# Kernel tuning notes

Hardware: AMD Instinct MI355X
Metric: run time of the kernel (lower is better)

The kernel has to match this reference:

```python
import jax, jax.numpy as jnp
import numpy as np

B, S, H, D = 2, 2048, 16, 64


def setup_inputs() -> dict:
    key = jax.random.key(0)
    kq, kk, kv, km = jax.random.split(key, 4)
    q = jax.random.normal(kq, (B, S, H, D), dtype=jnp.float32)
    k = jax.random.normal(kk, (B, S, H, D), dtype=jnp.float32)
    v = jax.random.normal(kv, (B, S, H, D), dtype=jnp.float32)
    key_padding_mask = jax.random.randint(km, (B, S), 0, 2).astype(bool)
    return {"q": q, "k": k, "v": v, "key_padding_mask": key_padding_mask}


def reference(q, k, v, key_padding_mask):
    # [B,S,H,D] -> [B,H,S,D]; fp32 upcast (inputs already fp32)
    qt = jnp.transpose(q, (0, 2, 1, 3)).astype(jnp.float32)
    kt = jnp.transpose(k, (0, 2, 1, 3)).astype(jnp.float32)
    vt = jnp.transpose(v, (0, 2, 1, 3)).astype(jnp.float32)
    scale = D ** (-0.5)
    # [B,H,Sq,Sk]
    scores = jnp.einsum("bhqd,bhkd->bhqk", qt, kt) * scale
    # masked_fill where key_padding_mask is True -> -inf
    mask = key_padding_mask[:, None, None, :]  # [B,1,1,Sk]
    scores = jnp.where(mask, -jnp.inf, scores)
    attn = jax.nn.softmax(scores, axis=-1)
    out = jnp.einsum("bhqk,bhkd->bhqd", attn, vt).astype(q.dtype)
    # back to [B,S,H,D]
    return jnp.transpose(out, (0, 2, 1, 3))
```

## Files before the change

kernel.cpp:

```cpp
#include <hip/hip_runtime.h>
#include <hip/hip_bf16.h>

#define BB 2
#define SS 2048
#define HH 16
#define DD 64
#define BR 128
#define BC 64
#define NT (SS / BC)
#define NQT (SS / BR)
#define TILE_E (BC * DD)
#define LOG2E 1.44269504f
#define LSTR 72

typedef __attribute__((ext_vector_type(8))) short short8;
typedef __attribute__((ext_vector_type(4))) float f32x4;
typedef __attribute__((ext_vector_type(16))) float f32x16;
typedef __attribute__((ext_vector_type(4))) unsigned int uint32x4;
typedef __attribute__((ext_vector_type(4))) unsigned short ushort4_t;

static __device__ __forceinline__ unsigned short f2bf(float f) {
    unsigned int u = __float_as_uint(f);
    unsigned int r = u + 0x7FFFu + ((u >> 16) & 1u);
    return (unsigned short)(r >> 16);
}
static __device__ __forceinline__ unsigned int pack2(float a, float b) {
    return (unsigned int)f2bf(a) | ((unsigned int)f2bf(b) << 16);
}
static __device__ __forceinline__ float fexp2(float x) {
#if __has_builtin(__builtin_amdgcn_exp2f)
    return __builtin_amdgcn_exp2f(x);
#else
    return exp2f(x);
#endif
}
static __device__ __forceinline__ void gl_lds16(const void* g, void* l) {
    __builtin_amdgcn_global_load_lds(
        (const __attribute__((address_space(1))) void*)g,
        (__attribute__((address_space(3))) void*)l, 16, 0, 0);
}

__global__ __launch_bounds__(256, 2)
void prep_kernel(const float* __restrict__ K, const float* __restrict__ V,
                 const int* __restrict__ M,
                 unsigned short* __restrict__ Kb, unsigned short* __restrict__ Vt,
                 unsigned long long* __restrict__ Mb64)
{
    __shared__ unsigned short Vl[DD * LSTR];

    const int t  = blockIdx.x & (NT - 1);
    const int b  = blockIdx.x >> 9;
    const int bh = blockIdx.x >> 5;
    const int tid = threadIdx.x;
    const size_t tile = (size_t)blockIdx.x * TILE_E;
    const size_t rs = (size_t)HH * DD;
    const float* kb0 = K + (((size_t)b * SS + t * BC) * HH + (bh & 15)) * DD;
    const float* vb0 = V + (((size_t)b * SS + t * BC) * HH + (bh & 15)) * DD;

    {
        const int p  = tid & 7;
        const int r0 = tid >> 3;
        #pragma unroll
        for (int half = 0; half < 2; ++half) {
            const int r = r0 + half * 32;
            const int c = p ^ (r & 7);
            const float* ks = kb0 + (size_t)r * rs + c * 8;
            const float4 f0 = *(const float4*)ks;
            const float4 f1 = *(const float4*)(ks + 4);
            short8 o;
            o[0] = (short)f2bf(f0.x); o[1] = (short)f2bf(f0.y);
            o[2] = (short)f2bf(f0.z); o[3] = (short)f2bf(f0.w);
            o[4] = (short)f2bf(f1.x); o[5] = (short)f2bf(f1.y);
            o[6] = (short)f2bf(f1.z); o[7] = (short)f2bf(f1.w);
            *(short8*)(Kb + tile + r * 64 + p * 8) = o;
        }
    }
    {
        const int vr = tid >> 2;
        const int vc = tid & 3;
        const float* vp = vb0 + (size_t)vr * rs + vc * 16;
        #pragma unroll
        for (int i = 0; i < 4; ++i) {
            const float4 f = *(const float4*)(vp + i * 4);
            const int d = vc * 16 + i * 4;
            Vl[(d + 0) * LSTR + vr] = f2bf(f.x);
            Vl[(d + 1) * LSTR + vr] = f2bf(f.y);
            Vl[(d + 2) * LSTR + vr] = f2bf(f.z);
            Vl[(d + 3) * LSTR + vr] = f2bf(f.w);
        }
    }
    __syncthreads();
    {
        const int p  = tid & 7;
        const int r0 = tid >> 3;
        #pragma unroll
        for (int half = 0; half < 2; ++half) {
            const int r = r0 + half * 32;
            const int c = p ^ (r & 7);
            const short8 o = *(const short8*)&Vl[r * LSTR + c * 8];
            *(short8*)(Vt + tile + r * 64 + p * 8) = o;
        }
    }
    if ((bh & 15) == 0 && tid < 64) {
        const int mv = M[(size_t)b * SS + t * BC + tid];
        const unsigned long long bal = __ballot(mv != 0);
        if (tid == 0) Mb64[(b << 5) + t] = bal;
    }
}

__global__ __launch_bounds__(256, 2)
void fa3_kernel(const float* __restrict__ Q,
                const unsigned short* __restrict__ Kb,
                const unsigned short* __restrict__ Vt,
                const unsigned long long* __restrict__ Mb64,
                float* __restrict__ O)
{
    __shared__ __align__(16) unsigned short Ks[2][TILE_E];
    __shared__ __align__(16) unsigned short Vs[2][TILE_E];

    const int blk = blockIdx.x;
    const int qt  = blk & (NQT - 1);
    const int bh  = blk >> 4;
    const int b   = bh >> 4;
    const int h   = bh & 15;

    const int tid  = threadIdx.x;
    const int wave = tid >> 6;
    const int lane = tid & 63;
    const int ln   = lane & 31;
    const int l5   = lane >> 5;

    const float qscale = 0.125f * LOG2E;
    const int qrow = qt * BR + wave * 32 + ln;
    const float* qp = Q + (((size_t)b * SS + qrow) * HH + h) * DD;
    short8 qf[4];
    #pragma unroll
    for (int t = 0; t < 4; ++t) {
        const int d0 = t * 16 + l5 * 8;
        const float4 f0 = *(const float4*)(qp + d0);
        const float4 f1 = *(const float4*)(qp + d0 + 4);
        short8 x;
        x[0] = (short)f2bf(f0.x * qscale); x[1] = (short)f2bf(f0.y * qscale);
        x[2] = (short)f2bf(f0.z * qscale); x[3] = (short)f2bf(f0.w * qscale);
        x[4] = (short)f2bf(f1.x * qscale); x[5] = (short)f2bf(f1.y * qscale);
        x[6] = (short)f2bf(f1.z * qscale); x[7] = (short)f2bf(f1.w * qscale);
        qf[t] = x;
    }

    f32x16 acc0, acc1;
    #pragma unroll
    for (int i = 0; i < 16; ++i) { acc0[i] = 0.f; acc1[i] = 0.f; }
    float lsum = 0.f;

    const unsigned short* kb_bh = Kb + (size_t)bh * NT * TILE_E;
    const unsigned short* vt_bh = Vt + (size_t)bh * NT * TILE_E;
    const int we = wave * 1024;
    const int wb = wave * 2048;

    gl_lds16(kb_bh + we + lane * 8,       (char*)Ks[0] + wb);
    gl_lds16(kb_bh + we + 512 + lane * 8, (char*)Ks[0] + wb + 1024);
    gl_lds16(vt_bh + we + lane * 8,       (char*)Vs[0] + wb);
    gl_lds16(vt_bh + we + 512 + lane * 8, (char*)Vs[0] + wb + 1024);
    __syncthreads();

    const int pswz = (ln & 7);

    for (int kt = 0; kt < NT; ++kt) {
        const int cur = kt & 1;
        const int nxt = cur ^ 1;
        const int kn = (kt + 1 < NT) ? kt + 1 : NT - 1;
        const unsigned short* kbt = kb_bh + (size_t)kn * TILE_E;
        const unsigned short* vtt = vt_bh + (size_t)kn * TILE_E;
        gl_lds16(kbt + we + lane * 8,       (char*)Ks[nxt] + wb);
        gl_lds16(kbt + we + 512 + lane * 8, (char*)Ks[nxt] + wb + 1024);
        gl_lds16(vtt + we + lane * 8,       (char*)Vs[nxt] + wb);
        gl_lds16(vtt + we + 512 + lane * 8, (char*)Vs[nxt] + wb + 1024);

        const unsigned long long mk = Mb64[(b << 5) + kt];
        const unsigned long long shm = mk >> (4 * l5);
        const unsigned int w0 = (unsigned int)shm;
        const unsigned int w1 = (unsigned int)(shm >> 32);

        f32x16 s0, s1;
        #pragma unroll
        for (int i = 0; i < 16; ++i) { s0[i] = 0.f; s1[i] = 0.f; }
        #pragma unroll
        for (int t = 0; t < 4; ++t) {
            const int p = (2 * t + l5) ^ pswz;
            const short8 kf0 = *(const short8*)(Ks[cur] + ln * 64 + p * 8);
            const short8 kf1 = *(const short8*)(Ks[cur] + (32 + ln) * 64 + p * 8);
            s0 = __builtin_amdgcn_mfma_f32_32x32x16_bf16(kf0, qf[t], s0, 0, 0, 0);
            s1 = __builtin_amdgcn_mfma_f32_32x32x16_bf16(kf1, qf[t], s1, 0, 0, 0);
        }

        unsigned int pk[2][8];
        #pragma unroll
        for (int hh = 0; hh < 2; ++hh) {
            const unsigned int w = hh ? w1 : w0;
            #pragma unroll
            for (int g = 0; g < 4; ++g) {
                float pv[4];
                #pragma unroll
                for (int j = 0; j < 4; ++j) {
                    float p = fexp2(hh ? s1[g * 4 + j] : s0[g * 4 + j]);
                    if ((w >> (8 * g + j)) & 1u) p = 0.f;
                    lsum += p;
                    pv[j] = p;
                }
                pk[hh][g * 2 + 0] = pack2(pv[0], pv[1]);
                pk[hh][g * 2 + 1] = pack2(pv[2], pv[3]);
            }
        }
        unsigned int xk[2][8];
        #pragma unroll
        for (int hh = 0; hh < 2; ++hh)
            #pragma unroll
            for (int i = 0; i < 8; ++i)
                xk[hh][i] = __shfl_xor(pk[hh][i], 32);

        short8 pf[4];
        #pragma unroll
        for (int t = 0; t < 4; ++t) {
            const int hh = t >> 1;
            const int s  = t & 1;
            uint32x4 u;
            u[0] = l5 ? xk[hh][(2 * s + 1) * 2]     : pk[hh][(2 * s) * 2];
            u[1] = l5 ? xk[hh][(2 * s + 1) * 2 + 1] : pk[hh][(2 * s) * 2 + 1];
            u[2] = l5 ? pk[hh][(2 * s + 1) * 2]     : xk[hh][(2 * s) * 2];
            u[3] = l5 ? pk[hh][(2 * s + 1) * 2 + 1] : xk[hh][(2 * s) * 2 + 1];
            pf[t] = __builtin_bit_cast(short8, u);
        }

        #pragma unroll
        for (int t = 0; t < 4; ++t) {
            const int p = (2 * t + l5) ^ pswz;
            const short8 vf0 = *(const short8*)(Vs[cur] + ln * 64 + p * 8);
            const short8 vf1 = *(const short8*)(Vs[cur] + (32 + ln) * 64 + p * 8);
            acc0 = __builtin_amdgcn_mfma_f32_32x32x16_bf16(vf0, pf[t], acc0, 0, 0, 0);
            acc1 = __builtin_amdgcn_mfma_f32_32x32x16_bf16(vf1, pf[t], acc1, 0, 0, 0);
        }

        __syncthreads();
    }

    const float l = lsum + __shfl_xor(lsum, 32);
    const float inv = 1.0f / l;
    float* op = O + (((size_t)b * SS + qrow) * HH + h) * DD;
    #pragma unroll
    for (int dh = 0; dh < 2; ++dh) {
        #pragma unroll
        for (int g = 0; g < 4; ++g) {
            const int d0 = dh * 32 + 8 * g + 4 * l5;
            float4 o;
            o.x = (dh ? acc1[g * 4 + 0] : acc0[g * 4 + 0]) * inv;
            o.y = (dh ? acc1[g * 4 + 1] : acc0[g * 4 + 1]) * inv;
            o.z = (dh ? acc1[g * 4 + 2] : acc0[g * 4 + 2]) * inv;
            o.w = (dh ? acc1[g * 4 + 3] : acc0[g * 4 + 3]) * inv;
            *(float4*)(op + d0) = o;
        }
    }
}

#define KP 72
#define FBR 64
__global__ __launch_bounds__(256, 2)
void fa_fallback(const float* __restrict__ Q, const float* __restrict__ K,
                 const float* __restrict__ V, const int* __restrict__ M,
                 float* __restrict__ O)
{
    __shared__ unsigned short KsF[BC][KP];
    __shared__ unsigned short VsF[DD][KP];
    __shared__ unsigned short PsF[4][16][KP];
    __shared__ float mb[BC];

    const int blk = blockIdx.x;
    const int qt = blk % (SS / FBR);
    const int bh = blk / (SS / FBR);
    const int b = bh / HH;
    const int h = bh % HH;
    const int tid = threadIdx.x;
    const int wave = tid >> 6;
    const int lane = tid & 63;
    const int lq = lane & 15;
    const int quad = lane >> 4;

    const int qrow = qt * FBR + wave * 16 + lq;
    const float* qp = Q + (((size_t)b * SS + qrow) * HH + h) * DD;
    short8 qf[2];
    #pragma unroll
    for (int c = 0; c < 2; ++c) {
        const float4 f0 = *(const float4*)(qp + c * 32 + quad * 8);
        const float4 f1 = *(const float4*)(qp + c * 32 + quad * 8 + 4);
        short8 t;
        t[0] = (short)f2bf(f0.x * 0.125f); t[1] = (short)f2bf(f0.y * 0.125f);
        t[2] = (short)f2bf(f0.z * 0.125f); t[3] = (short)f2bf(f0.w * 0.125f);
        t[4] = (short)f2bf(f1.x * 0.125f); t[5] = (short)f2bf(f1.y * 0.125f);
        t[6] = (short)f2bf(f1.z * 0.125f); t[7] = (short)f2bf(f1.w * 0.125f);
        qf[c] = t;
    }
    f32x4 acc[4];
    #pragma unroll
    for (int dt = 0; dt < 4; ++dt) acc[dt] = (f32x4){0.f, 0.f, 0.f, 0.f};
    float m_i[4] = {-1e30f, -1e30f, -1e30f, -1e30f};
    float l_i[4] = {0.f, 0.f, 0.f, 0.f};

    const int sr = tid >> 2;
    const int sc = tid & 3;
    const size_t rowstride = (size_t)HH * DD;
    const float* kbase = K + (((size_t)b * SS) * HH + h) * DD;
    const float* vbase = V + (((size_t)b * SS) * HH + h) * DD;

    for (int kt = 0; kt < NT; ++kt) {
        const int k0 = kt * BC;
        __syncthreads();
        {
            const float* kp = kbase + (size_t)(k0 + sr) * rowstride + sc * 16;
            #pragma unroll
            for (int i = 0; i < 4; ++i) {
                const float4 f = *(const float4*)(kp + i * 4);
                ushort4_t u;
                u[0] = f2bf(f.x); u[1] = f2bf(f.y); u[2] = f2bf(f.z); u[3] = f2bf(f.w);
                *(ushort4_t*)&KsF[sr][sc * 16 + i * 4] = u;
            }
            const float* vp = vbase + (size_t)(k0 + sr) * rowstride + sc * 16;
            #pragma unroll
            for (int i = 0; i < 4; ++i) {
                const float4 f = *(const float4*)(vp + i * 4);
                const int d = sc * 16 + i * 4;
                VsF[d + 0][sr] = f2bf(f.x); VsF[d + 1][sr] = f2bf(f.y);
                VsF[d + 2][sr] = f2bf(f.z); VsF[d + 3][sr] = f2bf(f.w);
            }
            if (tid < BC) mb[tid] = M[(size_t)b * SS + k0 + tid] ? -1e30f : 0.0f;
        }
        __syncthreads();
        f32x4 s[4];
        #pragma unroll
        for (int ct = 0; ct < 4; ++ct) {
            f32x4 z = (f32x4){0.f, 0.f, 0.f, 0.f};
            const unsigned short* kr = &KsF[ct * 16 + lq][quad * 8];
            const short8 kf0 = *(const short8*)kr;
            const short8 kf1 = *(const short8*)(kr + 32);
            z = __builtin_amdgcn_mfma_f32_16x16x32_bf16(qf[0], kf0, z, 0, 0, 0);
            z = __builtin_amdgcn_mfma_f32_16x16x32_bf16(qf[1], kf1, z, 0, 0, 0);
            s[ct] = z;
        }
        #pragma unroll
        for (int ct = 0; ct < 4; ++ct) {
            const float mbias = mb[ct * 16 + lq];
            s[ct][0] += mbias; s[ct][1] += mbias; s[ct][2] += mbias; s[ct][3] += mbias;
        }
        #pragma unroll
        for (int r = 0; r < 4; ++r) {
            float mx = fmaxf(fmaxf(s[0][r], s[1][r]), fmaxf(s[2][r], s[3][r]));
            mx = fmaxf(mx, __shfl_xor(mx, 1));
            mx = fmaxf(mx, __shfl_xor(mx, 2));
            mx = fmaxf(mx, __shfl_xor(mx, 4));
            mx = fmaxf(mx, __shfl_xor(mx, 8));
            const float m_new = fmaxf(m_i[r], mx);
            const float alpha = __expf(m_i[r] - m_new);
            m_i[r] = m_new;
            float rs = 0.f;
            #pragma unroll
            for (int ct = 0; ct < 4; ++ct) {
                const float p = __expf(s[ct][r] - m_new);
                rs += p;
                PsF[wave][quad * 4 + r][ct * 16 + lq] = f2bf(p);
            }
            rs += __shfl_xor(rs, 1); rs += __shfl_xor(rs, 2);
            rs += __shfl_xor(rs, 4); rs += __shfl_xor(rs, 8);
            l_i[r] = l_i[r] * alpha + rs;
            #pragma unroll
            for (int dt = 0; dt < 4; ++dt) acc[dt][r] *= alpha;
        }
        const unsigned short* pr = &PsF[wave][lq][quad * 8];
        const short8 pf0 = *(const short8*)pr;
        const short8 pf1 = *(const short8*)(pr + 32);
        #pragma unroll
        for (int dt = 0; dt < 4; ++dt) {
            const unsigned short* vr = &VsF[dt * 16 + lq][quad * 8];
            const short8 vf0 = *(const short8*)vr;
            const short8 vf1 = *(const short8*)(vr + 32);
            acc[dt] = __builtin_amdgcn_mfma_f32_16x16x32_bf16(pf0, vf0, acc[dt], 0, 0, 0);
            acc[dt] = __builtin_amdgcn_mfma_f32_16x16x32_bf16(pf1, vf1, acc[dt], 0, 0, 0);
        }
    }
    #pragma unroll
    for (int r = 0; r < 4; ++r) {
        const float inv = 1.0f / l_i[r];
        const int row = qt * FBR + wave * 16 + quad * 4 + r;
        float* op = O + (((size_t)b * SS + row) * HH + h) * DD;
        #pragma unroll
        for (int dt = 0; dt < 4; ++dt)
            op[dt * 16 + lq] = acc[dt][r] * inv;
    }
}

extern "C" void kernel_launch(void* const* d_in, const int* in_sizes, int n_in,
                              void* d_out, int out_size, void* d_ws, size_t ws_size,
                              hipStream_t stream) {
    const float* q = (const float*)d_in[0];
    const float* k = (const float*)d_in[1];
    const float* v = (const float*)d_in[2];
    const int*   m = (const int*)d_in[3];
    float* out = (float*)d_out;

    const int nprep = BB * HH * NT;
    const size_t kb_elems = (size_t)nprep * TILE_E;
    const size_t need = kb_elems * 2 * 2 + (size_t)BB * NT * 8;

    if (ws_size >= need) {
        unsigned short* Kb = (unsigned short*)d_ws;
        unsigned short* Vt = Kb + kb_elems;
        unsigned long long* Mb64 = (unsigned long long*)(Vt + kb_elems);
        prep_kernel<<<nprep, 256, 0, stream>>>(k, v, m, Kb, Vt, Mb64);
        fa3_kernel<<<BB * HH * NQT, 256, 0, stream>>>(q, Kb, Vt, Mb64, out);
    } else {
        fa_fallback<<<BB * HH * (SS / FBR), 256, 0, stream>>>(q, k, v, m, out);
    }
}
```

Baseline: 161.3 us.

## Split key range across two blocks per query tile and fold masking into K/V

New measurement: 153.1 us. 1.05x faster.

```diff
diff --git a/kernel.cpp b/kernel.cpp
--- a/kernel.cpp
+++ b/kernel.cpp
@@ -12,6 +12,7 @@
 #define TILE_E (BC * DD)
 #define LOG2E 1.44269504f
 #define LSTR 72
+#define OSZ (BB * SS * HH * DD)
 
 typedef __attribute__((ext_vector_type(8))) short short8;
 typedef __attribute__((ext_vector_type(4))) float f32x4;
@@ -44,7 +45,7 @@
 void prep_kernel(const float* __restrict__ K, const float* __restrict__ V,
                  const int* __restrict__ M,
                  unsigned short* __restrict__ Kb, unsigned short* __restrict__ Vt,
-                 unsigned long long* __restrict__ Mb64)
+                 int* __restrict__ mcnt)
 {
     __shared__ unsigned short Vl[DD * LSTR];
 
@@ -56,6 +57,7 @@
     const size_t rs = (size_t)HH * DD;
     const float* kb0 = K + (((size_t)b * SS + t * BC) * HH + (bh & 15)) * DD;
     const float* vb0 = V + (((size_t)b * SS + t * BC) * HH + (bh & 15)) * DD;
+    const int* mrow = M + (size_t)b * SS + t * BC;
 
     {
         const int p  = tid & 7;
@@ -64,29 +66,31 @@
         for (int half = 0; half < 2; ++half) {
             const int r = r0 + half * 32;
             const int c = p ^ (r & 7);
+            const float sel = mrow[r] ? 0.0f : 1.0f;
             const float* ks = kb0 + (size_t)r * rs + c * 8;
             const float4 f0 = *(const float4*)ks;
             const float4 f1 = *(const float4*)(ks + 4);
             short8 o;
-            o[0] = (short)f2bf(f0.x); o[1] = (short)f2bf(f0.y);
-            o[2] = (short)f2bf(f0.z); o[3] = (short)f2bf(f0.w);
-            o[4] = (short)f2bf(f1.x); o[5] = (short)f2bf(f1.y);
-            o[6] = (short)f2bf(f1.z); o[7] = (short)f2bf(f1.w);
+            o[0] = (short)f2bf(f0.x * sel); o[1] = (short)f2bf(f0.y * sel);
+            o[2] = (short)f2bf(f0.z * sel); o[3] = (short)f2bf(f0.w * sel);
+            o[4] = (short)f2bf(f1.x * sel); o[5] = (short)f2bf(f1.y * sel);
+            o[6] = (short)f2bf(f1.z * sel); o[7] = (short)f2bf(f1.w * sel);
             *(short8*)(Kb + tile + r * 64 + p * 8) = o;
         }
     }
     {
         const int vr = tid >> 2;
         const int vc = tid & 3;
+        const float sel = mrow[vr] ? 0.0f : 1.0f;
         const float* vp = vb0 + (size_t)vr * rs + vc * 16;
         #pragma unroll
         for (int i = 0; i < 4; ++i) {
             const float4 f = *(const float4*)(vp + i * 4);
             const int d = vc * 16 + i * 4;
-            Vl[(d + 0) * LSTR + vr] = f2bf(f.x);
-            Vl[(d + 1) * LSTR + vr] = f2bf(f.y);
-            Vl[(d + 2) * LSTR + vr] = f2bf(f.z);
-            Vl[(d + 3) * LSTR + vr] = f2bf(f.w);
+            Vl[(d + 0) * LSTR + vr] = f2bf(f.x * sel);
+            Vl[(d + 1) * LSTR + vr] = f2bf(f.y * sel);
+            Vl[(d + 2) * LSTR + vr] = f2bf(f.z * sel);
+            Vl[(d + 3) * LSTR + vr] = f2bf(f.w * sel);
         }
     }
     __syncthreads();
@@ -102,27 +106,31 @@
         }
     }
     if ((bh & 15) == 0 && tid < 64) {
-        const int mv = M[(size_t)b * SS + t * BC + tid];
-        const unsigned long long bal = __ballot(mv != 0);
-        if (tid == 0) Mb64[(b << 5) + t] = bal;
-    }
-}
-
+        const unsigned long long bal = __ballot(mrow[tid] != 0);
+        if (tid == 0) mcnt[b * NT + t] = (int)__popcll(bal);
+    }
+}
+
+template<bool SPLIT>
 __global__ __launch_bounds__(256, 2)
 void fa3_kernel(const float* __restrict__ Q,
                 const unsigned short* __restrict__ Kb,
                 const unsigned short* __restrict__ Vt,
-                const unsigned long long* __restrict__ Mb64,
-                float* __restrict__ O)
+                const int* __restrict__ mcnt,
+                float* __restrict__ Op,
+                float* __restrict__ Lp)
 {
     __shared__ __align__(16) unsigned short Ks[2][TILE_E];
     __shared__ __align__(16) unsigned short Vs[2][TILE_E];
 
     const int blk = blockIdx.x;
     const int qt  = blk & (NQT - 1);
-    const int bh  = blk >> 4;
+    const int bh  = (blk >> 4) & 31;
+    const int spl = SPLIT ? (blk >> 9) : 0;
     const int b   = bh >> 4;
     const int h   = bh & 15;
+    const int kt0 = SPLIT ? spl * (NT / 2) : 0;
+    const int ktn = SPLIT ? (NT / 2) : NT;
 
     const int tid  = threadIdx.x;
     const int wave = tid >> 6;
@@ -147,6 +155,9 @@
         qf[t] = x;
     }
 
+    int corr = 0;
+    for (int i = 0; i < ktn; ++i) corr += mcnt[b * NT + kt0 + i];
+
     f32x16 acc0, acc1;
     #pragma unroll
     for (int i = 0; i < 16; ++i) { acc0[i] = 0.f; acc1[i] = 0.f; }
@@ -157,18 +168,22 @@
     const int we = wave * 1024;
     const int wb = wave * 2048;
 
-    gl_lds16(kb_bh + we + lane * 8,       (char*)Ks[0] + wb);
-    gl_lds16(kb_bh + we + 512 + lane * 8, (char*)Ks[0] + wb + 1024);
-    gl_lds16(vt_bh + we + lane * 8,       (char*)Vs[0] + wb);
-    gl_lds16(vt_bh + we + 512 + lane * 8, (char*)Vs[0] + wb + 1024);
+    {
+        const unsigned short* kbt = kb_bh + (size_t)kt0 * TILE_E;
+        const unsigned short* vtt = vt_bh + (size_t)kt0 * TILE_E;
+        gl_lds16(kbt + we + lane * 8,       (char*)Ks[0] + wb);
+        gl_lds16(kbt + we + 512 + lane * 8, (char*)Ks[0] + wb + 1024);
+        gl_lds16(vtt + we + lane * 8,       (char*)Vs[0] + wb);
+        gl_lds16(vtt + we + 512 + lane * 8, (char*)Vs[0] + wb + 1024);
+    }
     __syncthreads();
 
     const int pswz = (ln & 7);
 
-    for (int kt = 0; kt < NT; ++kt) {
-        const int cur = kt & 1;
+    for (int it = 0; it < ktn; ++it) {
+        const int cur = it & 1;
         const int nxt = cur ^ 1;
-        const int kn = (kt + 1 < NT) ? kt + 1 : NT - 1;
+        const int kn = kt0 + ((it + 1 < ktn) ? it + 1 : it);
         const unsigned short* kbt = kb_bh + (size_t)kn * TILE_E;
         const unsigned short* vtt = vt_bh + (size_t)kn * TILE_E;
         gl_lds16(kbt + we + lane * 8,       (char*)Ks[nxt] + wb);
@@ -176,11 +191,6 @@
         gl_lds16(vtt + we + lane * 8,       (char*)Vs[nxt] + wb);
         gl_lds16(vtt + we + 512 + lane * 8, (char*)Vs[nxt] + wb + 1024);
 
-        const unsigned long long mk = Mb64[(b << 5) + kt];
-        const unsigned long long shm = mk >> (4 * l5);
-        const unsigned int w0 = (unsigned int)shm;
-        const unsigned int w1 = (unsigned int)(shm >> 32);
-
         f32x16 s0, s1;
         #pragma unroll
         for (int i = 0; i < 16; ++i) { s0[i] = 0.f; s1[i] = 0.f; }
@@ -196,14 +206,12 @@
         unsigned int pk[2][8];
         #pragma unroll
         for (int hh = 0; hh < 2; ++hh) {
-            const unsigned int w = hh ? w1 : w0;
             #pragma unroll
             for (int g = 0; g < 4; ++g) {
                 float pv[4];
                 #pragma unroll
                 for (int j = 0; j < 4; ++j) {
-                    float p = fexp2(hh ? s1[g * 4 + j] : s0[g * 4 + j]);
-                    if ((w >> (8 * g + j)) & 1u) p = 0.f;
+                    const float p = fexp2(hh ? s1[g * 4 + j] : s0[g * 4 + j]);
                     lsum += p;
                     pv[j] = p;
                 }
@@ -243,22 +251,63 @@
         __syncthreads();
     }
 
-    const float l = lsum + __shfl_xor(lsum, 32);
+    const float l = lsum + __shfl_xor(lsum, 32) - (float)corr;
+    if (SPLIT) {
+        float* op = Op + (size_t)spl * OSZ + (((size_t)b * SS + qrow) * HH + h) * DD;
+        #pragma unroll
+        for (int dh = 0; dh < 2; ++dh) {
+            #pragma unroll
+            for (int g = 0; g < 4; ++g) {
+                const int d0 = dh * 32 + 8 * g + 4 * l5;
+                float4 o;
+                o.x = dh ? acc1[g * 4 + 0] : acc0[g * 4 + 0];
+                o.y = dh ? acc1[g * 4 + 1] : acc0[g * 4 + 1];
+                o.z = dh ? acc1[g * 4 + 2] : acc0[g * 4 + 2];
+                o.w = dh ? acc1[g * 4 + 3] : acc0[g * 4 + 3];
+                *(float4*)(op + d0) = o;
+            }
+        }
+        if (l5 == 0)
+            Lp[spl * (BB * HH * SS) + (b * HH + h) * SS + qrow] = l;
+    } else {
+        const float inv = 1.0f / l;
+        float* op = Op + (((size_t)b * SS + qrow) * HH + h) * DD;
+        #pragma unroll
+        for (int dh = 0; dh < 2; ++dh) {
+            #pragma unroll
+            for (int g = 0; g < 4; ++g) {
+                const int d0 = dh * 32 + 8 * g + 4 * l5;
+                float4 o;
+                o.x = (dh ? acc1[g * 4 + 0] : acc0[g * 4 + 0]) * inv;
+                o.y = (dh ? acc1[g * 4 + 1] : acc0[g * 4 + 1]) * inv;
+                o.z = (dh ? acc1[g * 4 + 2] : acc0[g * 4 + 2]) * inv;
+                o.w = (dh ? acc1[g * 4 + 3] : acc0[g * 4 + 3]) * inv;
+                *(float4*)(op + d0) = o;
+            }
+        }
+    }
+}
+
+__global__ __launch_bounds__(256, 4)
+void combine_kernel(const float* __restrict__ Ou, const float* __restrict__ Lp,
+                    float* __restrict__ O)
+{
+    const int gid = blockIdx.x * 256 + threadIdx.x;
+    const int i = gid * 4;
+    const int b   = i >> 21;
+    const int row = (i >> 10) & (SS - 1);
+    const int h   = (i >> 6) & (HH - 1);
+    const int li  = (b * HH + h) * SS + row;
+    const float l = Lp[li] + Lp[BB * HH * SS + li];
     const float inv = 1.0f / l;
-    float* op = O + (((size_t)b * SS + qrow) * HH + h) * DD;
-    #pragma unroll
-    for (int dh = 0; dh < 2; ++dh) {
-        #pragma unroll
-        for (int g = 0; g < 4; ++g) {
-            const int d0 = dh * 32 + 8 * g + 4 * l5;
-            float4 o;
-            o.x = (dh ? acc1[g * 4 + 0] : acc0[g * 4 + 0]) * inv;
-            o.y = (dh ? acc1[g * 4 + 1] : acc0[g * 4 + 1]) * inv;
-            o.z = (dh ? acc1[g * 4 + 2] : acc0[g * 4 + 2]) * inv;
-            o.w = (dh ? acc1[g * 4 + 3] : acc0[g * 4 + 3]) * inv;
-            *(float4*)(op + d0) = o;
-        }
-    }
+    const float4 a = *(const float4*)(Ou + i);
+    const float4 c = *(const float4*)(Ou + OSZ + i);
+    float4 o;
+    o.x = (a.x + c.x) * inv;
+    o.y = (a.y + c.y) * inv;
+    o.z = (a.z + c.z) * inv;
+    o.w = (a.w + c.w) * inv;
+    *(float4*)(O + i) = o;
 }
 
 #define KP 72
@@ -405,15 +454,32 @@
     float* out = (float*)d_out;
 
     const int nprep = BB * HH * NT;
-    const size_t kb_elems = (size_t)nprep * TILE_E;
-    const size_t need = kb_elems * 2 * 2 + (size_t)BB * NT * 8;
-
-    if (ws_size >= need) {
+    const size_t kb_bytes = (size_t)nprep * TILE_E * 2;
+    const size_t ou_bytes = (size_t)2 * OSZ * 4;
+    const size_t lp_bytes = (size_t)2 * BB * HH * SS * 4;
+    const size_t mc_bytes = (size_t)BB * NT * 4;
+
+    const size_t need_split  = 2 * kb_bytes + ou_bytes + lp_bytes + mc_bytes;
+    const size_t need_single = 2 * kb_bytes + mc_bytes;
+
+    if (ws_size >= need_single) {
         unsigned short* Kb = (unsigned short*)d_ws;
-        unsigned short* Vt = Kb + kb_elems;
-        unsigned long long* Mb64 = (unsigned long long*)(Vt + kb_elems);
-        prep_kernel<<<nprep, 256, 0, stream>>>(k, v, m, Kb, Vt, Mb64);
-        fa3_kernel<<<BB * HH * NQT, 256, 0, stream>>>(q, Kb, Vt, Mb64, out);
+        unsigned short* Vt = (unsigned short*)((char*)d_ws + kb_bytes);
+        char* rest = (char*)d_ws + 2 * kb_bytes;
+        if (ws_size >= need_split) {
+            float* Ou = (float*)rest;
+            float* Lp = (float*)(rest + ou_bytes);
+            int* mcnt = (int*)(rest + ou_bytes + lp_bytes);
+            prep_kernel<<<nprep, 256, 0, stream>>>(k, v, m, Kb, Vt, mcnt);
+            fa3_kernel<true><<<2 * BB * HH * NQT, 256, 0, stream>>>(
+                q, Kb, Vt, mcnt, Ou, Lp);
+            combine_kernel<<<OSZ / 4 / 256, 256, 0, stream>>>(Ou, Lp, out);
+        } else {
+            int* mcnt = (int*)rest;
+            prep_kernel<<<nprep, 256, 0, stream>>>(k, v, m, Kb, Vt, mcnt);
+            fa3_kernel<false><<<BB * HH * NQT, 256, 0, stream>>>(
+                q, Kb, Vt, mcnt, out, nullptr);
+        }
     } else {
         fa_fallback<<<BB * HH * (SS / FBR), 256, 0, stream>>>(q, k, v, m, out);
     }
```
